# Performance work log

Hardware: AMD Instinct MI355X
Metric: run time of the kernel (lower is better)

## Reference

```python
import jax, jax.numpy as jnp
import numpy as np

B, Q, D = 4, 1024, 1024
N, DH = 16, 64  # n_head, d_head
SCALE = 1.0 / DH ** 0.5
LN_EPS = 1e-5


def setup_inputs() -> dict:
    key = jax.random.key(0)
    ks = jax.random.split(key, 10)
    return {
        "w": jax.random.normal(ks[0], (B, Q, D), jnp.float32),
        "r_emb": jax.random.normal(ks[1], (Q, N, DH), jnp.float32),
        "r_w_bias": jax.random.normal(ks[2], (N, DH), jnp.float32),
        "r_bias": jax.random.normal(ks[3], (Q, N), jnp.float32),
        # projection weights stored [in, out]; torch Linear init std = 1/sqrt(d_head)
        "Wq": jax.random.normal(ks[4], (D, N * DH), jnp.float32) * SCALE,
        "Wk": jax.random.normal(ks[5], (D, N * DH), jnp.float32) * SCALE,
        "Wv": jax.random.normal(ks[6], (D, N * DH), jnp.float32) * SCALE,
        "Wo": jax.random.normal(ks[7], (N * DH, D), jnp.float32) * SCALE,
        "ln_gamma": jnp.ones((D,), jnp.float32),
        "ln_beta": jnp.zeros((D,), jnp.float32),
    }


def _rel_shift(x):
    # x: [b, i, j, n]; pad a zero column at the end of j then drop j=0
    # equivalent to shifting left by one along j with a trailing zero.
    return jnp.concatenate([x[:, :, 1:, :], jnp.zeros_like(x[:, :, :1, :])], axis=2)


def reference(w, r_emb, r_w_bias, r_bias, Wq, Wk, Wv, Wo, ln_gamma, ln_beta):
    b, qlen, d = w.shape
    klen = qlen  # mems=None
    n, dh = r_w_bias.shape

    q_h = (w @ Wq).reshape(b, qlen, n, dh)
    k_h = (w @ Wk).reshape(b, klen, n, dh)
    v_h = (w @ Wv).reshape(b, klen, n, dh)

    rw_q = q_h + r_w_bias[None, None]                      # [b,q,n,dh]
    AC = jnp.einsum('bind,bjnd->bijn', rw_q, k_h)          # [b,q,k,n]
    B_ = jnp.einsum('bind,jnd->bijn', q_h, r_emb)          # [b,q,k,n]
    BD = _rel_shift(B_ + r_bias[None, None])               # [b,q,k,n]

    attn_score = (AC + BD) * SCALE
    attn_prob = jax.nn.softmax(attn_score, axis=2)
    attn_vec = jnp.einsum('bijn,bjnd->bind', attn_prob, v_h)
    attn_out = attn_vec.reshape(b, qlen, n * dh) @ Wo

    out = w + attn_out  # residual (post-lnorm path)
    mu = jnp.mean(out, axis=-1, keepdims=True)
    var = jnp.var(out, axis=-1, keepdims=True)
    return (out - mu) / jnp.sqrt(var + LN_EPS) * ln_gamma + ln_beta
```

## Files before the change

### kernel.cpp

```cpp
#include <hip/hip_runtime.h>
#include <hip/hip_bf16.h>

using f16 = _Float16;
typedef _Float16 f16x8 __attribute__((ext_vector_type(8)));
typedef _Float16 f16x4 __attribute__((ext_vector_type(4)));
typedef float f32x4 __attribute__((ext_vector_type(4)));

#define AS1 __attribute__((address_space(1)))
#define AS3 __attribute__((address_space(3)))

constexpr int Bc = 4, Qc = 1024, Dc = 1024, Nh = 16, DHc = 64;
constexpr int BQ = Bc * Qc;
constexpr int NHEAD = Bc * Nh;
constexpr float ATT_SCALE = 0.125f;
constexpr float LOG2E = 1.44269504088896f;

struct Ptr4 { const float* p[4]; };
__global__ __launch_bounds__(256) void k_prep(
    const float* __restrict__ w_in, f16* __restrict__ wh,
    Ptr4 srcs, f16* __restrict__ WT,
    const float* __restrict__ remb, f16* __restrict__ Ke)
{
    const int bid = blockIdx.x, tid = threadIdx.x;
    if (bid < 2048) {
        long i8 = ((long)bid * 256 + tid) * 8;
        float4 a = *(const float4*)&w_in[i8];
        float4 b = *(const float4*)&w_in[i8 + 4];
        f16x8 o = { (f16)a.x, (f16)a.y, (f16)a.z, (f16)a.w,
                    (f16)b.x, (f16)b.y, (f16)b.z, (f16)b.w };
        *(f16x8*)&wh[i8] = o;
    } else if (bid < 6144) {
        __shared__ f16 tile[32][33];
        int idx = bid - 2048;
        int z = idx >> 10, rem = idx & 1023;
        int r0 = (rem >> 5) * 32, c0 = (rem & 31) * 32;
        const float* src = srcs.p[z];
        f16* d = WT + (long)z * Dc * Dc;
        int tx = tid & 31, ty = tid >> 5;
#pragma unroll
        for (int dy = 0; dy < 32; dy += 8) {
            int r = r0 + ty + dy, c = c0 + tx;
            tile[ty + dy][tx] = (f16)src[(long)r * Dc + c];
        }
        __syncthreads();
#pragma unroll
        for (int dy = 0; dy < 32; dy += 8) {
            int c = c0 + ty + dy, r = r0 + tx;
            d[(long)c * Dc + r] = tile[tx][ty + dy];
        }
    } else {
        long gid = (long)(bid - 6144) * 256 + tid;
        int d8 = (int)(gid & 7) * 8;
        int j = (int)((gid >> 3) & 1023);
        int h = (int)(gid >> 13);
        int n = h & 15;
        f16x8 kv;
        if (j < 1023) {
            const float* rp = &remb[((long)(j + 1) * 16 + n) * 64 + d8];
            float4 r0 = *(const float4*)rp, r1 = *(const float4*)(rp + 4);
            kv[0] = (f16)r0.x; kv[1] = (f16)r0.y; kv[2] = (f16)r0.z; kv[3] = (f16)r0.w;
            kv[4] = (f16)r1.x; kv[5] = (f16)r1.y; kv[6] = (f16)r1.z; kv[7] = (f16)r1.w;
        } else {
            kv = f16x8{};
        }
        *(f16x8*)&Ke[(((long)h << 10) + j) * 64 + d8] = kv;
    }
}

template <int BM, int BN, int BK, int WROWS, int WCOLS, int EPI>
__global__ __launch_bounds__(256) void k_gemm_nt(
    const f16* __restrict__ A, const f16* __restrict__ Bt, void* __restrict__ Cv,
    f16* __restrict__ qtp, f16* __restrict__ ktp, f16* __restrict__ vtp,
    int lda, int ldb, int ldc, int K)
{
    static_assert(BK == 64, "geometry below assumes BK=64");
    constexpr int TM = BM / (WROWS * 16);
    constexpr int TN = BN / (WCOLS * 16);
    __shared__ __align__(16) f16 sA[BM * 64];
    __shared__ __align__(16) f16 sB[BN * 64];

    const int tid = threadIdx.x;
    const int lane = tid & 63, wave = tid >> 6;
    const int wm = wave / WCOLS, wn = wave % WCOLS;

    const int nwg = gridDim.x * gridDim.y;
    const int flat = blockIdx.y * gridDim.x + blockIdx.x;
    const int cpx = nwg >> 3;
    const int swz = (flat & 7) * cpx + (flat >> 3);
    const int bx = swz % gridDim.x, by = swz / gridDim.x;
    const int m0 = by * BM, n0 = bx * BN;

    f32x4 acc[TM][TN] = {};

    const int lrow = lane & 15;
    const int quad = lane >> 4;
    const int srow = lane >> 3;
    const int scol = ((lane & 7) ^ (srow & 7)) * 8;

    for (int k0 = 0; k0 < K; k0 += 64) {
        __syncthreads();
        constexpr int CHA = BM / 8;
#pragma unroll
        for (int ch = 0; ch < CHA / 4; ++ch) {
            int cc = ch * 4 + wave;
            __builtin_amdgcn_global_load_lds(
                (const AS1 void*)(const void*)&A[(long)(m0 + cc * 8 + srow) * lda + k0 + scol],
                (AS3 void*)(void*)&sA[cc * 512], 16, 0, 0);
        }
        constexpr int CHB = BN / 8;
#pragma unroll
        for (int ch = 0; ch < CHB / 4; ++ch) {
            int cc = ch * 4 + wave;
            __builtin_amdgcn_global_load_lds(
                (const AS1 void*)(const void*)&Bt[(long)(n0 + cc * 8 + srow) * ldb + k0 + scol],
                (AS3 void*)(void*)&sB[cc * 512], 16, 0, 0);
        }
        __syncthreads();

#pragma unroll
        for (int kk = 0; kk < 2; ++kk) {
            const int kcb = kk * 4 + quad;
            f16x8 af[TM], bfr[TN];
#pragma unroll
            for (int mi = 0; mi < TM; ++mi) {
                int R = wm * TM * 16 + mi * 16 + lrow;
                af[mi] = *(const f16x8*)&sA[R * 64 + ((kcb ^ (lrow & 7)) * 8)];
            }
#pragma unroll
            for (int ni = 0; ni < TN; ++ni) {
                int R = wn * TN * 16 + ni * 16 + lrow;
                bfr[ni] = *(const f16x8*)&sB[R * 64 + ((kcb ^ (lrow & 7)) * 8)];
            }
#pragma unroll
            for (int mi = 0; mi < TM; ++mi)
#pragma unroll
                for (int ni = 0; ni < TN; ++ni)
                    acc[mi][ni] = __builtin_amdgcn_mfma_f32_16x16x32_f16(af[mi], bfr[ni], acc[mi][ni], 0, 0, 0);
        }
    }

    const int crow = (lane >> 4) * 4;
    const int ccol = lane & 15;
#pragma unroll
    for (int mi = 0; mi < TM; ++mi)
#pragma unroll
        for (int ni = 0; ni < TN; ++ni)
#pragma unroll
            for (int r = 0; r < 4; ++r) {
                int gm = m0 + wm * TM * 16 + mi * 16 + crow + r;
                int gn = n0 + wn * TN * 16 + ni * 16 + ccol;
                float val = acc[mi][ni][r];
                if constexpr (EPI == 0) {
                    ((f16*)Cv)[(long)gm * ldc + gn] = (f16)val;
                } else {
                    int seg = n0 >> 10;
                    int col = gn & 1023;
                    if (seg == 0) {
                        qtp[(long)gm * 1024 + col] = (f16)val;
                    } else if (seg == 1) {
                        ktp[(long)gm * 1024 + col] = (f16)val;
                    } else {
                        int b = gm >> 10, i = gm & 1023;
                        vtp[(((long)(b << 10) + col) << 10) + i] = (f16)val;
                    }
                }
            }
}

__global__ __launch_bounds__(512, 4) void k_flash(
    const f16* __restrict__ qh, const f16* __restrict__ kh,
    const f16* __restrict__ Ke, const f16* __restrict__ vT,
    const float* __restrict__ rwb, const float* __restrict__ r_bias,
    f16* __restrict__ avp)
{
    __shared__ __align__(16) f16 sKa[2][64 * 64];
    __shared__ __align__(16) f16 sKe[2][64 * 64];
    __shared__ __align__(16) f16 sVa[2][64 * 64];
    __shared__ float sRB[2][64];

    const int tid = threadIdx.x, lane = tid & 63, wave = tid >> 6;
    const int bid = blockIdx.x;
    const int h = (((bid >> 3) & 7) << 3) | (bid & 7);
    const int i0 = (bid >> 6) * 128;
    const int b = h >> 4, n = h & 15;

    const int lrow = lane & 15;
    const int quad = lane >> 4;
    const int lr3 = lane >> 3;
    const int swc = (lane & 7) ^ (lr3 & 7);

    const f16* srcK = kh + ((long)(b * Qc) + 8 * wave + lr3) * 1024 + n * 64 + swc * 8;
    const f16* srcE = Ke + ((long)h * Qc + 8 * wave + lr3) * 64 + swc * 8;
    const f16* srcV = vT + (long)h * DHc * Qc + (long)(8 * wave + lr3) * Qc + swc * 8;

    f16x8 rw0, rw1;
#pragma unroll
    for (int e = 0; e < 8; ++e) {
        rw0[e] = (f16)(rwb[n * 64 + quad * 8 + e] * ATT_SCALE);
        rw1[e] = (f16)(rwb[n * 64 + 32 + quad * 8 + e] * ATT_SCALE);
    }

    const f16 qsc = (f16)0.125f;
    f16x8 aq[4];
    {
        long rix = (long)(b * Qc + i0 + wave * 16 + lrow) * 1024 + n * 64;
        f16x8 q0 = *(const f16x8*)&qh[rix + quad * 8] * qsc;
        f16x8 q1 = *(const f16x8*)&qh[rix + 32 + quad * 8] * qsc;
        aq[0] = q0 + rw0;
        aq[1] = q1 + rw1;
        aq[2] = q0;
        aq[3] = q1;
    }

    float m_i = -1e30f, l_i = 0.0f;
    f32x4 o_acc[4] = {};

    {
        float rbv = 0.0f;
        if (tid < 64) rbv = r_bias[(tid + 1) * Nh + n] * (ATT_SCALE * LOG2E);
        __builtin_amdgcn_global_load_lds((const AS1 void*)srcK, (AS3 void*)&sKa[0][wave * 512], 16, 0, 0);
        __builtin_amdgcn_global_load_lds((const AS1 void*)srcE, (AS3 void*)&sKe[0][wave * 512], 16, 0, 0);
        __builtin_amdgcn_global_load_lds((const AS1 void*)srcV, (AS3 void*)&sVa[0][wave * 512], 16, 0, 0);
        if (tid < 64) sRB[0][tid] = rbv;
    }
    __syncthreads();

    for (int jt = 0; jt < 16; ++jt) {
        const int cur = jt & 1;

        float rbn = 0.0f;
        if (jt < 15) {
            const int j0n = (jt + 1) * 64;
            __builtin_amdgcn_global_load_lds((const AS1 void*)(srcK + (long)j0n * 1024),
                                             (AS3 void*)&sKa[cur ^ 1][wave * 512], 16, 0, 0);
            __builtin_amdgcn_global_load_lds((const AS1 void*)(srcE + (long)j0n * 64),
                                             (AS3 void*)&sKe[cur ^ 1][wave * 512], 16, 0, 0);
            __builtin_amdgcn_global_load_lds((const AS1 void*)(srcV + j0n),
                                             (AS3 void*)&sVa[cur ^ 1][wave * 512], 16, 0, 0);
            if (tid < 64) {
                int j = j0n + tid;
                rbn = (j < Qc - 1) ? r_bias[(j + 1) * Nh + n] * (ATT_SCALE * LOG2E) : 0.0f;
            }
        }

        const f16* Ka = &sKa[cur][0];
        const f16* Kb = &sKe[cur][0];
        const f16* Va = &sVa[cur][0];
        const int rsw = lrow & 7;

        f32x4 s_acc[4] = {};
        __builtin_amdgcn_s_setprio(1);
#pragma unroll
        for (int ni = 0; ni < 4; ++ni) {
            int rb_ = (ni * 16 + lrow) * 64;
            f16x8 a0 = *(const f16x8*)&Ka[rb_ + ((0 + quad) ^ rsw) * 8];
            f16x8 a1 = *(const f16x8*)&Ka[rb_ + ((4 + quad) ^ rsw) * 8];
            f16x8 e0 = *(const f16x8*)&Kb[rb_ + ((0 + quad) ^ rsw) * 8];
            f16x8 e1 = *(const f16x8*)&Kb[rb_ + ((4 + quad) ^ rsw) * 8];
            s_acc[ni] = __builtin_amdgcn_mfma_f32_16x16x32_f16(a0, aq[0], s_acc[ni], 0, 0, 0);
            s_acc[ni] = __builtin_amdgcn_mfma_f32_16x16x32_f16(a1, aq[1], s_acc[ni], 0, 0, 0);
            s_acc[ni] = __builtin_amdgcn_mfma_f32_16x16x32_f16(e0, aq[2], s_acc[ni], 0, 0, 0);
            s_acc[ni] = __builtin_amdgcn_mfma_f32_16x16x32_f16(e1, aq[3], s_acc[ni], 0, 0, 0);
        }
        __builtin_amdgcn_s_setprio(0);

        f16x4 pf[4];
        float mx = -1e30f, sm = 0.0f;
#pragma unroll
        for (int ni = 0; ni < 4; ++ni) {
            f32x4 rb4 = *(const f32x4*)&sRB[cur][ni * 16 + quad * 4];
            f16x4 pvv;
#pragma unroll
            for (int r = 0; r < 4; ++r) {
                float v = fmaf(s_acc[ni][r], LOG2E, rb4[r]);
                s_acc[ni][r] = v;
                mx = fmaxf(mx, v);
                float e = __builtin_amdgcn_exp2f(v - m_i);
                sm += e;
                pvv[r] = (f16)e;
            }
            pf[ni] = pvv;
        }
        if (!__all(mx - m_i <= 8.0f)) {
            float wmx = fmaxf(mx, __shfl_xor(mx, 16));
            wmx = fmaxf(wmx, __shfl_xor(wmx, 32));
            float mn = fmaxf(m_i, wmx);
            float alpha = __builtin_amdgcn_exp2f(m_i - mn);
            sm = 0.0f;
#pragma unroll
            for (int ni = 0; ni < 4; ++ni) {
                f16x4 pvv;
#pragma unroll
                for (int r = 0; r < 4; ++r) {
                    float e = __builtin_amdgcn_exp2f(s_acc[ni][r] - mn);
                    sm += e;
                    pvv[r] = (f16)e;
                }
                pf[ni] = pvv;
            }
            l_i *= alpha;
#pragma unroll
            for (int r = 0; r < 4; ++r) {
                float al = __shfl(alpha, quad * 4 + r);
#pragma unroll
                for (int dt = 0; dt < 4; ++dt) o_acc[dt][r] *= al;
            }
            m_i = mn;
        }
        l_i += sm;

        __builtin_amdgcn_s_setprio(1);
#pragma unroll
        for (int nj = 0; nj < 4; ++nj) {
            int coff = ((2 * nj + (quad >> 1)) ^ rsw) * 8 + (quad & 1) * 4;
#pragma unroll
            for (int dt = 0; dt < 4; ++dt) {
                f16x4 bv = *(const f16x4*)&Va[(dt * 16 + lrow) * 64 + coff];
                o_acc[dt] = __builtin_amdgcn_mfma_f32_16x16x16f16(pf[nj], bv, o_acc[dt], 0, 0, 0);
            }
        }
        __builtin_amdgcn_s_setprio(0);

        if (jt < 15) {
            if (tid < 64) sRB[cur ^ 1][tid] = rbn;
            __syncthreads();
        }
    }

    l_i += __shfl_xor(l_i, 16);
    l_i += __shfl_xor(l_i, 32);
    {
        float linv = 1.0f / l_i;
#pragma unroll
        for (int r = 0; r < 4; ++r) {
            float li = __shfl(linv, quad * 4 + r);
            int i = i0 + wave * 16 + quad * 4 + r;
#pragma unroll
            for (int dt = 0; dt < 4; ++dt) {
                int d = dt * 16 + lrow;
                avp[((long)(b * Qc + i) << 10) + n * 64 + d] = (f16)(o_acc[dt][r] * li);
            }
        }
    }
}

__global__ __launch_bounds__(256) void k_res_ln(const float* __restrict__ w, const f16* __restrict__ ao,
                                                const float* __restrict__ gamma, const float* __restrict__ beta,
                                                float* __restrict__ out) {
    const long base = (long)blockIdx.x * 1024;
    const int tid = threadIdx.x;
    float4 wv = *(const float4*)&w[base + tid * 4];
    f16x4 av = *(const f16x4*)&ao[base + tid * 4];
    float x[4] = { wv.x + (float)av[0], wv.y + (float)av[1],
                   wv.z + (float)av[2], wv.w + (float)av[3] };
    float s = x[0] + x[1] + x[2] + x[3];
    float s2 = x[0] * x[0] + x[1] * x[1] + x[2] * x[2] + x[3] * x[3];
#pragma unroll
    for (int off = 32; off; off >>= 1) { s += __shfl_down(s, off); s2 += __shfl_down(s2, off); }
    __shared__ float rs[4], rs2[4];
    if ((tid & 63) == 0) { rs[tid >> 6] = s; rs2[tid >> 6] = s2; }
    __syncthreads();
    s = rs[0] + rs[1] + rs[2] + rs[3];
    s2 = rs2[0] + rs2[1] + rs2[2] + rs2[3];
    float mu = s * (1.0f / 1024.0f);
    float var = s2 * (1.0f / 1024.0f) - mu * mu;
    float inv = rsqrtf(var + 1e-5f);
    float4 gv = *(const float4*)&gamma[tid * 4];
    float4 bv = *(const float4*)&beta[tid * 4];
    float4 o;
    o.x = (x[0] - mu) * inv * gv.x + bv.x;
    o.y = (x[1] - mu) * inv * gv.y + bv.y;
    o.z = (x[2] - mu) * inv * gv.z + bv.z;
    o.w = (x[3] - mu) * inv * gv.w + bv.w;
    *(float4*)&out[base + tid * 4] = o;
}

extern "C" void kernel_launch(void* const* d_in, const int* in_sizes, int n_in,
                              void* d_out, int out_size, void* d_ws, size_t ws_size,
                              hipStream_t stream) {
    const float* w_in   = (const float*)d_in[0];
    const float* r_emb  = (const float*)d_in[1];
    const float* r_wb   = (const float*)d_in[2];
    const float* r_bias = (const float*)d_in[3];
    const float* Wq     = (const float*)d_in[4];
    const float* Wk     = (const float*)d_in[5];
    const float* Wv     = (const float*)d_in[6];
    const float* Wo     = (const float*)d_in[7];
    const float* ln_g   = (const float*)d_in[8];
    const float* ln_b   = (const float*)d_in[9];
    float* out = (float*)d_out;

    char* p = (char*)d_ws;
    auto alloc = [&](size_t bytes) { char* r = p; p += (bytes + 255) & ~(size_t)255; return r; };
    f16* wh = (f16*)alloc((size_t)BQ * Dc * 2);
    f16* WT = (f16*)alloc((size_t)4 * Dc * Dc * 2);
    f16* qh = (f16*)alloc((size_t)BQ * Dc * 2);
    f16* kh = (f16*)alloc((size_t)BQ * Dc * 2);
    f16* Ke = (f16*)alloc((size_t)NHEAD * Qc * DHc * 2);
    f16* vT = (f16*)alloc((size_t)BQ * Dc * 2);
    f16* WoT = WT + (size_t)3 * Dc * Dc;
    f16* avp = wh;
    f16* ao  = Ke;

    Ptr4 srcs{{Wq, Wk, Wv, Wo}};
    k_prep<<<8192, 256, 0, stream>>>(w_in, wh, srcs, WT, r_emb, Ke);

    k_gemm_nt<128, 128, 64, 2, 2, 5><<<dim3(3 * Dc / 128, BQ / 128), 256, 0, stream>>>(
        wh, WT, nullptr, qh, kh, vT, Dc, Dc, 0, Dc);

    k_flash<<<512, 512, 0, stream>>>(qh, kh, Ke, vT, r_wb, r_bias, avp);

    k_gemm_nt<64, 128, 64, 2, 2, 0><<<dim3(Dc / 128, BQ / 64), 256, 0, stream>>>(
        avp, WoT, ao, nullptr, nullptr, nullptr, Dc, Dc, Dc, Dc);

    k_res_ln<<<BQ, 256, 0, stream>>>(w_in, ao, ln_g, ln_b, out);
}
```

Before: 207.9 us.

## Double-buffer GEMM LDS tiles with BK=32 to overlap loads and MFMA

Restructures the NT GEMM main loop to use two LDS buffers of K-depth 32. The next tile's global_load_lds is issued before computing on the current tile, with one barrier per iteration instead of two. A new XOR swizzle is added for the 32-wide rows. This aims to hide global-to-LDS latency behind MFMA work, at the cost of twice as many loop iterations and barriers. It also relies on the barrier correctly waiting for the async LDS loads.

```diff
diff --git a/kernel.cpp b/kernel.cpp
--- a/kernel.cpp
+++ b/kernel.cpp
@@ -73,11 +73,11 @@
     f16* __restrict__ qtp, f16* __restrict__ ktp, f16* __restrict__ vtp,
     int lda, int ldb, int ldc, int K)
 {
-    static_assert(BK == 64, "geometry below assumes BK=64");
+    static_assert(BK == 32, "geometry below assumes BK=32 double-buffered");
     constexpr int TM = BM / (WROWS * 16);
     constexpr int TN = BN / (WCOLS * 16);
-    __shared__ __align__(16) f16 sA[BM * 64];
-    __shared__ __align__(16) f16 sB[BN * 64];
+    __shared__ __align__(16) f16 sA[2][BM * 32];
+    __shared__ __align__(16) f16 sB[2][BN * 32];
 
     const int tid = threadIdx.x;
     const int lane = tid & 63, wave = tid >> 6;
@@ -94,49 +94,56 @@
 
     const int lrow = lane & 15;
     const int quad = lane >> 4;
-    const int srow = lane >> 3;
-    const int scol = ((lane & 7) ^ (srow & 7)) * 8;
-
-    for (int k0 = 0; k0 < K; k0 += 64) {
-        __syncthreads();
-        constexpr int CHA = BM / 8;
+    const int srow = lane >> 2;
+    const int scol = ((lane & 3) ^ ((srow >> 1) & 3)) * 8;
+    const int rsw2 = (lrow >> 1) & 3;
+
+    auto stage = [&](int buf, int k0) {
+        constexpr int CHA = BM / 16;
 #pragma unroll
         for (int ch = 0; ch < CHA / 4; ++ch) {
             int cc = ch * 4 + wave;
             __builtin_amdgcn_global_load_lds(
-                (const AS1 void*)(const void*)&A[(long)(m0 + cc * 8 + srow) * lda + k0 + scol],
-                (AS3 void*)(void*)&sA[cc * 512], 16, 0, 0);
-        }
-        constexpr int CHB = BN / 8;
+                (const AS1 void*)(const void*)&A[(long)(m0 + cc * 16 + srow) * lda + k0 + scol],
+                (AS3 void*)(void*)&sA[buf][cc * 512], 16, 0, 0);
+        }
+        constexpr int CHB = BN / 16;
 #pragma unroll
         for (int ch = 0; ch < CHB / 4; ++ch) {
             int cc = ch * 4 + wave;
             __builtin_amdgcn_global_load_lds(
-                (const AS1 void*)(const void*)&Bt[(long)(n0 + cc * 8 + srow) * ldb + k0 + scol],
-                (AS3 void*)(void*)&sB[cc * 512], 16, 0, 0);
-        }
-        __syncthreads();
-
-#pragma unroll
-        for (int kk = 0; kk < 2; ++kk) {
-            const int kcb = kk * 4 + quad;
-            f16x8 af[TM], bfr[TN];
-#pragma unroll
-            for (int mi = 0; mi < TM; ++mi) {
-                int R = wm * TM * 16 + mi * 16 + lrow;
-                af[mi] = *(const f16x8*)&sA[R * 64 + ((kcb ^ (lrow & 7)) * 8)];
-            }
-#pragma unroll
-            for (int ni = 0; ni < TN; ++ni) {
-                int R = wn * TN * 16 + ni * 16 + lrow;
-                bfr[ni] = *(const f16x8*)&sB[R * 64 + ((kcb ^ (lrow & 7)) * 8)];
-            }
-#pragma unroll
-            for (int mi = 0; mi < TM; ++mi)
-#pragma unroll
-                for (int ni = 0; ni < TN; ++ni)
-                    acc[mi][ni] = __builtin_amdgcn_mfma_f32_16x16x32_f16(af[mi], bfr[ni], acc[mi][ni], 0, 0, 0);
-        }
+                (const AS1 void*)(const void*)&Bt[(long)(n0 + cc * 16 + srow) * ldb + k0 + scol],
+                (AS3 void*)(void*)&sB[buf][cc * 512], 16, 0, 0);
+        }
+    };
+
+    stage(0, 0);
+    __syncthreads();
+
+    const int NKT = K / 32;
+    for (int kt = 0; kt < NKT; ++kt) {
+        const int cur = kt & 1;
+        if (kt + 1 < NKT) stage(cur ^ 1, (kt + 1) * 32);
+
+        f16x8 af[TM], bfr[TN];
+#pragma unroll
+        for (int mi = 0; mi < TM; ++mi) {
+            int R = wm * TM * 16 + mi * 16 + lrow;
+            af[mi] = *(const f16x8*)&sA[cur][R * 32 + (quad ^ rsw2) * 8];
+        }
+#pragma unroll
+        for (int ni = 0; ni < TN; ++ni) {
+            int R = wn * TN * 16 + ni * 16 + lrow;
+            bfr[ni] = *(const f16x8*)&sB[cur][R * 32 + (quad ^ rsw2) * 8];
+        }
+#pragma unroll
+        for (int mi = 0; mi < TM; ++mi)
+#pragma unroll
+            for (int ni = 0; ni < TN; ++ni)
+                acc[mi][ni] = __builtin_amdgcn_mfma_f32_16x16x32_f16(af[mi], bfr[ni], acc[mi][ni], 0, 0, 0);
+
+        if (kt + 1 < NKT)
+            __syncthreads();
     }
 
     const int crow = (lane >> 4) * 4;
@@ -405,12 +412,12 @@
     Ptr4 srcs{{Wq, Wk, Wv, Wo}};
     k_prep<<<8192, 256, 0, stream>>>(w_in, wh, srcs, WT, r_emb, Ke);
 
-    k_gemm_nt<128, 128, 64, 2, 2, 5><<<dim3(3 * Dc / 128, BQ / 128), 256, 0, stream>>>(
+    k_gemm_nt<128, 128, 32, 2, 2, 5><<<dim3(3 * Dc / 128, BQ / 128), 256, 0, stream>>>(
         wh, WT, nullptr, qh, kh, vT, Dc, Dc, 0, Dc);
 
     k_flash<<<512, 512, 0, stream>>>(qh, kh, Ke, vT, r_wb, r_bias, avp);
 
-    k_gemm_nt<64, 128, 64, 2, 2, 0><<<dim3(Dc / 128, BQ / 64), 256, 0, stream>>>(
+    k_gemm_nt<64, 128, 32, 2, 2, 0><<<dim3(Dc / 128, BQ / 64), 256, 0, stream>>>(
         avp, WoT, ao, nullptr, nullptr, nullptr, Dc, Dc, Dc, Dc);
 
     k_res_ln<<<BQ, 256, 0, stream>>>(w_in, ao, ln_g, ln_b, out);
```

New measurement: 203.4 us. 1.02x faster.
